# Optimization experiments

Measured on AMD Instinct MI355X. Metric: run time of the kernel, lower is better.

The kernel has to match this reference:

```python
import jax, jax.numpy as jnp
import numpy as np

IN_FEATURES = 1024
OUT_FEATURES = 32000
PADDING_IDX = 0
SMOOTHING = 0.1
N_TOKENS = 8192


def setup_inputs() -> dict:
    key = jax.random.key(0)
    k_x, k_t, k_w, k_b = jax.random.split(key, 4)
    x = jax.random.normal(k_x, (N_TOKENS, IN_FEATURES), dtype=jnp.float32)
    target = jax.random.randint(k_t, (N_TOKENS,), 0, OUT_FEATURES, dtype=jnp.int64)
    # nn.init.uniform_(w, -0.1, 0.1) for both weight and bias
    weight = jax.random.uniform(k_w, (OUT_FEATURES, IN_FEATURES), dtype=jnp.float32, minval=-0.1, maxval=0.1)
    bias = jax.random.uniform(k_b, (OUT_FEATURES,), dtype=jnp.float32, minval=-0.1, maxval=0.1)
    return {"input": x, "target": target, "weight": weight, "bias": bias}


def reference(input, target, weight, bias):
    # Fused linear -> log-softmax -> label-smoothed NLL with padding mask.
    # logits: [N, V]
    logits = jnp.einsum("nd,vd->nv", input, weight) + bias
    logp = jax.nn.log_softmax(logits, axis=-1)
    V = logp.shape[-1]
    nll = -jnp.take_along_axis(logp, target[:, None], axis=-1)[:, 0]  # [N]
    smooth = -jnp.sum(logp, axis=-1)                                   # [N]
    per_tok = (1.0 - SMOOTHING) * nll + (SMOOTHING / V) * smooth
    mask = (target != PADDING_IDX).astype(per_tok.dtype)
    return jnp.sum(per_tok * mask)
```

## Files before the change

### kernel.cpp

```cpp
#include <hip/hip_runtime.h>

#define IN_F 1024
#define NVOC 32000
#define NTOK 8192
#define BM 128
#define BN 128
#define NT (NVOC / BN)
#define MT (NTOK / BM)
#define NBLK (NT * MT)
#define SMOOTH 0.1f

typedef __attribute__((ext_vector_type(8))) short short8;
typedef __attribute__((ext_vector_type(4))) float f32x4;
typedef __attribute__((ext_vector_type(8))) int int8v;
typedef __attribute__((ext_vector_type(4))) int int4v;
typedef unsigned int u32;

__device__ inline unsigned short f2bf(float f) {
  u32 u = __float_as_uint(f);
  return (unsigned short)((u + 0x7fffu + ((u >> 16) & 1u)) >> 16);
}

__device__ inline void gload_lds16(const void* g, void* l) {
  __builtin_amdgcn_global_load_lds(
      (const __attribute__((address_space(1))) u32*)g,
      (__attribute__((address_space(3))) u32*)l, 16, 0, 0);
}

__global__ void fix_target(const int* __restrict__ traw, int* __restrict__ tgtidx) {
  __shared__ int flag;
  if (threadIdx.x == 0) flag = 0;
  __syncthreads();
  int any = 0;
  for (int i = threadIdx.x; i < NTOK / 2; i += 256) any |= (traw[2 * i + 1] != 0);
  if (any) atomicOr(&flag, 1);
  __syncthreads();
  const int is64 = (flag == 0);
  for (int i = threadIdx.x; i < NTOK; i += 256)
    tgtidx[i] = is64 ? traw[2 * i] : traw[i];
}

__global__ void convert_fp8(const float4* __restrict__ in, u32* __restrict__ out, int n4) {
  int i = blockIdx.x * blockDim.x + threadIdx.x;
  const int stride = gridDim.x * blockDim.x;
  for (; i < n4; i += stride) {
    const float4 v = in[i];
    int p = __builtin_amdgcn_cvt_pk_fp8_f32(v.x, v.y, 0, false);
    p = __builtin_amdgcn_cvt_pk_fp8_f32(v.z, v.w, p, true);
    out[i] = (u32)p;
  }
}

__global__ __launch_bounds__(256) void gemm_fp8(
    const char* __restrict__ X8, const char* __restrict__ W8,
    const float* __restrict__ bias, const int* __restrict__ tgtidx,
    float* __restrict__ psum, float* __restrict__ pslog,
    float* __restrict__ tgtlogit) {
  __shared__ char smem[33792];
  char* As = smem;
  char* Bs = smem + 16384;
  float* biasS = (float*)(smem + 32768);
  int* tgtS = (int*)(smem + 33280);
  float* redse = (float*)smem;
  float* redsl = (float*)(smem + 1024);

  const int tid = threadIdx.x;
  const int wave = tid >> 6, lane = tid & 63;
  const int wm = wave & 1, wn = wave >> 1;
  const int quad = lane >> 4, l16 = lane & 15;

  const int lid = blockIdx.x;
  const int xcd = lid & 7, seq = lid >> 3;
  const int mt = (xcd << 3) | (seq & 7);
  const int nb = seq >> 3;
  const int n0 = nb * BN, m0 = mt * BM;

  if (tid < BN) {
    biasS[tid] = bias[n0 + tid];
    tgtS[tid] = tgtidx[m0 + tid] - n0;
  }

  const f32x4 zero = {0.f, 0.f, 0.f, 0.f};
  f32x4 acc[4][4];
#pragma unroll
  for (int i = 0; i < 4; ++i)
#pragma unroll
    for (int j = 0; j < 4; ++j) acc[i][j] = zero;

  const int lr = lane >> 3, lc = lane & 7;
  const char* pA[4];
  const char* pB[4];
#pragma unroll
  for (int i = 0; i < 4; ++i) {
    const int row = wave * 32 + i * 8 + lr;
    const int c = lc ^ (row & 7);
    pA[i] = X8 + (size_t)(m0 + row) * IN_F + c * 16;
    pB[i] = W8 + (size_t)(n0 + row) * IN_F + c * 16;
  }

  for (int kt = 0; kt < IN_F / 128; ++kt) {
    __syncthreads();
#pragma unroll
    for (int i = 0; i < 4; ++i) {
      const int R0 = wave * 32 + i * 8;
      gload_lds16(pA[i], As + R0 * 128);
      gload_lds16(pB[i], Bs + R0 * 128);
      pA[i] += 128;
      pB[i] += 128;
    }
    __syncthreads();

    int8v bfv[4];
#pragma unroll
    for (int t = 0; t < 4; ++t) {
      const int br = wn * 64 + t * 16 + l16;
      const int s0 = (((quad << 1) + 0) ^ (br & 7)) << 4;
      const int s1 = (((quad << 1) + 1) ^ (br & 7)) << 4;
      const int4v lo = *(const int4v*)(Bs + br * 128 + s0);
      const int4v hi = *(const int4v*)(Bs + br * 128 + s1);
      int8v f;
      f[0] = lo[0]; f[1] = lo[1]; f[2] = lo[2]; f[3] = lo[3];
      f[4] = hi[0]; f[5] = hi[1]; f[6] = hi[2]; f[7] = hi[3];
      bfv[t] = f;
    }
#pragma unroll
    for (int i = 0; i < 4; ++i) {
      const int ar = wm * 64 + i * 16 + l16;
      const int s0 = (((quad << 1) + 0) ^ (ar & 7)) << 4;
      const int s1 = (((quad << 1) + 1) ^ (ar & 7)) << 4;
      const int4v lo = *(const int4v*)(As + ar * 128 + s0);
      const int4v hi = *(const int4v*)(As + ar * 128 + s1);
      int8v af;
      af[0] = lo[0]; af[1] = lo[1]; af[2] = lo[2]; af[3] = lo[3];
      af[4] = hi[0]; af[5] = hi[1]; af[6] = hi[2]; af[7] = hi[3];
#pragma unroll
      for (int j = 0; j < 4; ++j)
        acc[i][j] = __builtin_amdgcn_mfma_scale_f32_16x16x128_f8f6f4(
            af, bfv[j], acc[i][j], 0 , 0 ,
            0, 0x7F7F7F7F, 0, 0x7F7F7F7F);
    }
  }

  __syncthreads();

  const float bv0 = biasS[wn * 64 + 0 * 16 + l16];
  const float bv1 = biasS[wn * 64 + 1 * 16 + l16];
  const float bv2 = biasS[wn * 64 + 2 * 16 + l16];
  const float bv3 = biasS[wn * 64 + 3 * 16 + l16];

#pragma unroll
  for (int i = 0; i < 4; ++i) {
#pragma unroll
    for (int reg = 0; reg < 4; ++reg) {
      const int row = wm * 64 + i * 16 + quad * 4 + reg;
      const float v0 = acc[i][0][reg] + bv0;
      const float v1 = acc[i][1][reg] + bv1;
      const float v2 = acc[i][2][reg] + bv2;
      const float v3 = acc[i][3][reg] + bv3;
      float se = __expf(v0) + __expf(v1) + __expf(v2) + __expf(v3);
      float sl = v0 + v1 + v2 + v3;
      se += __shfl_xor(se, 1); se += __shfl_xor(se, 2);
      se += __shfl_xor(se, 4); se += __shfl_xor(se, 8);
      sl += __shfl_xor(sl, 1); sl += __shfl_xor(sl, 2);
      sl += __shfl_xor(sl, 4); sl += __shfl_xor(sl, 8);
      if (l16 == 0) {
        redse[wn * 128 + row] = se;
        redsl[wn * 128 + row] = sl;
      }
      const int ct = tgtS[row];
      if (ct >= 0 && ct < BN && (ct >> 6) == wn && (ct & 15) == l16) {
        const int jj = (ct >> 4) & 3;
        const float tv = jj == 0 ? v0 : (jj == 1 ? v1 : (jj == 2 ? v2 : v3));
        tgtlogit[m0 + row] = tv;
      }
    }
  }
  __syncthreads();
  if (tid < BM) {
    const size_t idx = (size_t)(m0 + tid) * NT + nb;
    psum[idx] = redse[tid] + redse[128 + tid];
    pslog[idx] = redsl[tid] + redsl[128 + tid];
  }
}

__global__ __launch_bounds__(256) void gemm_fb(
    const float* __restrict__ X, const float* __restrict__ W,
    const float* __restrict__ bias, const int* __restrict__ tgtidx,
    float* __restrict__ psum, float* __restrict__ pslog,
    float* __restrict__ tgtlogit) {
  __shared__ char smem[33792];
  char* As = smem;
  char* Bs = smem + 16384;
  float* biasS = (float*)(smem + 32768);
  int* tgtS = (int*)(smem + 33280);
  float* redse = (float*)smem;
  float* redsl = (float*)(smem + 1024);

  const int tid = threadIdx.x;
  const int wave = tid >> 6, lane = tid & 63;
  const int wm = wave & 1, wn = wave >> 1;
  const int quad = lane >> 4, l16 = lane & 15;
  const int lid = blockIdx.x;
  const int xcd = lid & 7, seq = lid >> 3;
  const int mt = (xcd << 3) | (seq & 7);
  const int nb = seq >> 3;
  const int n0 = nb * BN, m0 = mt * BM;

  if (tid < BN) {
    biasS[tid] = bias[n0 + tid];
    tgtS[tid] = tgtidx[m0 + tid] - n0;
  }

  const f32x4 zero = {0.f, 0.f, 0.f, 0.f};
  f32x4 acc[4][4];
#pragma unroll
  for (int i = 0; i < 4; ++i)
#pragma unroll
    for (int j = 0; j < 4; ++j) acc[i][j] = zero;

  for (int kt = 0; kt < IN_F / 64; ++kt) {
    const int row = tid >> 1, hs = tid & 1;
    const float4* gA = (const float4*)(X + (size_t)(m0 + row) * IN_F + kt * 64 + hs * 32);
    const float4* gB = (const float4*)(W + (size_t)(n0 + row) * IN_F + kt * 64 + hs * 32);
    float4 a4[8], b4[8];
#pragma unroll
    for (int k = 0; k < 8; ++k) a4[k] = gA[k];
#pragma unroll
    for (int k = 0; k < 8; ++k) b4[k] = gB[k];
    __syncthreads();
#pragma unroll
    for (int cl = 0; cl < 4; ++cl) {
      const float4 x0 = a4[2 * cl], x1 = a4[2 * cl + 1];
      const float4 y0 = b4[2 * cl], y1 = b4[2 * cl + 1];
      short8 sa, sb;
      sa[0] = (short)f2bf(x0.x); sa[1] = (short)f2bf(x0.y);
      sa[2] = (short)f2bf(x0.z); sa[3] = (short)f2bf(x0.w);
      sa[4] = (short)f2bf(x1.x); sa[5] = (short)f2bf(x1.y);
      sa[6] = (short)f2bf(x1.z); sa[7] = (short)f2bf(x1.w);
      sb[0] = (short)f2bf(y0.x); sb[1] = (short)f2bf(y0.y);
      sb[2] = (short)f2bf(y0.z); sb[3] = (short)f2bf(y0.w);
      sb[4] = (short)f2bf(y1.x); sb[5] = (short)f2bf(y1.y);
      sb[6] = (short)f2bf(y1.z); sb[7] = (short)f2bf(y1.w);
      const int c = hs * 4 + cl;
      const int p = (c ^ (row & 7)) << 4;
      *(short8*)(As + row * 128 + p) = sa;
      *(short8*)(Bs + row * 128 + p) = sb;
    }
    __syncthreads();
#pragma unroll
    for (int kk = 0; kk < 2; ++kk) {
      short8 af[4], bfv[4];
#pragma unroll
      for (int t = 0; t < 4; ++t) {
        const int ar = wm * 64 + t * 16 + l16;
        af[t] = *(const short8*)(As + ar * 128 + ((((kk << 2) + quad) ^ (ar & 7)) << 4));
        const int br = wn * 64 + t * 16 + l16;
        bfv[t] = *(const short8*)(Bs + br * 128 + ((((kk << 2) + quad) ^ (br & 7)) << 4));
      }
#pragma unroll
      for (int i = 0; i < 4; ++i)
#pragma unroll
        for (int j = 0; j < 4; ++j)
          acc[i][j] = __builtin_amdgcn_mfma_f32_16x16x32_bf16(af[i], bfv[j], acc[i][j], 0, 0, 0);
    }
  }

  __syncthreads();
  const float bv0 = biasS[wn * 64 + 0 * 16 + l16];
  const float bv1 = biasS[wn * 64 + 1 * 16 + l16];
  const float bv2 = biasS[wn * 64 + 2 * 16 + l16];
  const float bv3 = biasS[wn * 64 + 3 * 16 + l16];
#pragma unroll
  for (int i = 0; i < 4; ++i) {
#pragma unroll
    for (int reg = 0; reg < 4; ++reg) {
      const int row = wm * 64 + i * 16 + quad * 4 + reg;
      const float v0 = acc[i][0][reg] + bv0;
      const float v1 = acc[i][1][reg] + bv1;
      const float v2 = acc[i][2][reg] + bv2;
      const float v3 = acc[i][3][reg] + bv3;
      float se = __expf(v0) + __expf(v1) + __expf(v2) + __expf(v3);
      float sl = v0 + v1 + v2 + v3;
      se += __shfl_xor(se, 1); se += __shfl_xor(se, 2);
      se += __shfl_xor(se, 4); se += __shfl_xor(se, 8);
      sl += __shfl_xor(sl, 1); sl += __shfl_xor(sl, 2);
      sl += __shfl_xor(sl, 4); sl += __shfl_xor(sl, 8);
      if (l16 == 0) {
        redse[wn * 128 + row] = se;
        redsl[wn * 128 + row] = sl;
      }
      const int ct = tgtS[row];
      if (ct >= 0 && ct < BN && (ct >> 6) == wn && (ct & 15) == l16) {
        const int jj = (ct >> 4) & 3;
        const float tv = jj == 0 ? v0 : (jj == 1 ? v1 : (jj == 2 ? v2 : v3));
        tgtlogit[m0 + row] = tv;
      }
    }
  }
  __syncthreads();
  if (tid < BM) {
    const size_t idx = (size_t)(m0 + tid) * NT + nb;
    psum[idx] = redse[tid] + redse[128 + tid];
    pslog[idx] = redsl[tid] + redsl[128 + tid];
  }
}

__global__ __launch_bounds__(256) void combine(
    const float* __restrict__ psum, const float* __restrict__ pslog,
    const float* __restrict__ tgtlogit, const int* __restrict__ tgtidx,
    float* __restrict__ pertok) {
  const int token = blockIdx.x * 4 + (threadIdx.x >> 6);
  const int lane = threadIdx.x & 63;
  float se = 0.f, sl = 0.f;
  for (int l = lane; l < NT; l += 64) {
    const size_t idx = (size_t)token * NT + l;
    se += psum[idx];
    sl += pslog[idx];
  }
#pragma unroll
  for (int d = 1; d < 64; d <<= 1) {
    se += __shfl_xor(se, d);
    sl += __shfl_xor(sl, d);
  }
  if (lane == 0) {
    const int t = tgtidx[token];
    const float logZ = logf(se);
    const float nll = logZ - tgtlogit[token];
    const float smooth = (float)NVOC * logZ - sl;
    const float pt = (1.f - SMOOTH) * nll + (SMOOTH / (float)NVOC) * smooth;
    pertok[token] = (t != 0) ? pt : 0.f;
  }
}

__global__ __launch_bounds__(256) void finalsum(const float* __restrict__ pertok,
                                                float* __restrict__ out) {
  const int tid = threadIdx.x;
  float s = 0.f;
  for (int i = tid; i < NTOK; i += 256) s += pertok[i];
#pragma unroll
  for (int d = 1; d < 64; d <<= 1) s += __shfl_xor(s, d);
  __shared__ float wsum[4];
  if ((tid & 63) == 0) wsum[tid >> 6] = s;
  __syncthreads();
  if (tid == 0) out[0] = wsum[0] + wsum[1] + wsum[2] + wsum[3];
}

extern "C" void kernel_launch(void* const* d_in, const int* in_sizes, int n_in,
                              void* d_out, int out_size, void* d_ws, size_t ws_size,
                              hipStream_t stream) {
  (void)in_sizes; (void)n_in; (void)out_size;
  const float* x = (const float*)d_in[0];
  const int* traw = (const int*)d_in[1];
  const float* w = (const float*)d_in[2];
  const float* bias = (const float*)d_in[3];

  char* ws = (char*)d_ws;
  float* psum = (float*)ws;
  float* pslog = psum + (size_t)NTOK * NT;
  float* tgtlogit = pslog + (size_t)NTOK * NT;
  float* pertok = tgtlogit + NTOK;
  int* tgtidx = (int*)(pertok + NTOK);
  char* fraw = (char*)(tgtidx + NTOK);
  char* f8base = (char*)(((size_t)fraw + 15) & ~(size_t)15);
  const size_t base_need = (size_t)(f8base - ws);
  const size_t f8_need = (size_t)NTOK * IN_F + (size_t)NVOC * IN_F;
  const bool pre8 = ws_size >= base_need + f8_need;

  fix_target<<<1, 256, 0, stream>>>(traw, tgtidx);

  if (pre8) {
    char* x8 = f8base;
    char* w8 = x8 + (size_t)NTOK * IN_F;
    convert_fp8<<<2048, 256, 0, stream>>>((const float4*)x, (u32*)x8, NTOK * IN_F / 4);
    convert_fp8<<<8192, 256, 0, stream>>>((const float4*)w, (u32*)w8, NVOC * IN_F / 4);
    gemm_fp8<<<NBLK, 256, 0, stream>>>(x8, w8, bias, tgtidx, psum, pslog, tgtlogit);
  } else {
    gemm_fb<<<NBLK, 256, 0, stream>>>(x, w, bias, tgtidx, psum, pslog, tgtlogit);
  }
  combine<<<NTOK / 4, 256, 0, stream>>>(psum, pslog, tgtlogit, tgtidx, pertok);
  finalsum<<<1, 256, 0, stream>>>(pertok, (float*)d_out);
}
```

Before: 666.7 us.

## Fuse prep kernels, fold final sum into combine, adjust LDS swizzle and occupancy

Merges the target fix-up and both FP8 conversion launches into a single prep kernel, and replaces the separate final-sum kernel with an atomicAdd at the end of combine, preceded by a memset of the output. The GEMM gets a launch-bounds occupancy hint of 3 blocks per SM, and the LDS chunk mapping now pairs chunks quad and quad+4 instead of 2*quad and 2*quad+1. The aim is fewer launches and fewer LDS bank conflicts. The trade-offs are a floating-point atomic reduction whose summation order is not fixed, and possible register spilling under the tighter occupancy bound.

New measurement: 740.1 us. +11.0%, slower.

```diff
diff --git a/kernel.cpp b/kernel.cpp
--- a/kernel.cpp
+++ b/kernel.cpp
@@ -27,31 +27,38 @@
       (__attribute__((address_space(3))) u32*)l, 16, 0, 0);
 }
 
-__global__ void fix_target(const int* __restrict__ traw, int* __restrict__ tgtidx) {
-  __shared__ int flag;
-  if (threadIdx.x == 0) flag = 0;
-  __syncthreads();
-  int any = 0;
-  for (int i = threadIdx.x; i < NTOK / 2; i += 256) any |= (traw[2 * i + 1] != 0);
-  if (any) atomicOr(&flag, 1);
-  __syncthreads();
-  const int is64 = (flag == 0);
-  for (int i = threadIdx.x; i < NTOK; i += 256)
-    tgtidx[i] = is64 ? traw[2 * i] : traw[i];
-}
-
-__global__ void convert_fp8(const float4* __restrict__ in, u32* __restrict__ out, int n4) {
-  int i = blockIdx.x * blockDim.x + threadIdx.x;
-  const int stride = gridDim.x * blockDim.x;
-  for (; i < n4; i += stride) {
-    const float4 v = in[i];
+__global__ void prep(const float4* __restrict__ x, const float4* __restrict__ w,
+                     u32* __restrict__ x8, u32* __restrict__ w8,
+                     const int* __restrict__ traw, int* __restrict__ tgtidx) {
+  if (blockIdx.x == 0) {
+    __shared__ int flag;
+    if (threadIdx.x == 0) flag = 0;
+    __syncthreads();
+    int any = 0;
+    for (int i = threadIdx.x; i < NTOK / 2; i += 256) any |= (traw[2 * i + 1] != 0);
+    if (any) atomicOr(&flag, 1);
+    __syncthreads();
+    const int is64 = (flag == 0);
+    for (int i = threadIdx.x; i < NTOK; i += 256)
+      tgtidx[i] = is64 ? traw[2 * i] : traw[i];
+  }
+  const int gid = blockIdx.x * 256 + threadIdx.x;
+  const int stride = gridDim.x * 256;
+  for (int i = gid; i < NTOK * IN_F / 4; i += stride) {
+    const float4 v = x[i];
     int p = __builtin_amdgcn_cvt_pk_fp8_f32(v.x, v.y, 0, false);
     p = __builtin_amdgcn_cvt_pk_fp8_f32(v.z, v.w, p, true);
-    out[i] = (u32)p;
-  }
-}
-
-__global__ __launch_bounds__(256) void gemm_fp8(
+    x8[i] = (u32)p;
+  }
+  for (int i = gid; i < NVOC * IN_F / 4; i += stride) {
+    const float4 v = w[i];
+    int p = __builtin_amdgcn_cvt_pk_fp8_f32(v.x, v.y, 0, false);
+    p = __builtin_amdgcn_cvt_pk_fp8_f32(v.z, v.w, p, true);
+    w8[i] = (u32)p;
+  }
+}
+
+__global__ __launch_bounds__(256, 3) void gemm_fp8(
     const char* __restrict__ X8, const char* __restrict__ W8,
     const float* __restrict__ bias, const int* __restrict__ tgtidx,
     float* __restrict__ psum, float* __restrict__ pslog,
@@ -93,7 +100,8 @@
 #pragma unroll
   for (int i = 0; i < 4; ++i) {
     const int row = wave * 32 + i * 8 + lr;
-    const int c = lc ^ (row & 7);
+    const int u = lc ^ (row & 7);
+    const int c = ((u & 3) << 1) | (u >> 2);
     pA[i] = X8 + (size_t)(m0 + row) * IN_F + c * 16;
     pB[i] = W8 + (size_t)(n0 + row) * IN_F + c * 16;
   }
@@ -114,8 +122,8 @@
 #pragma unroll
     for (int t = 0; t < 4; ++t) {
       const int br = wn * 64 + t * 16 + l16;
-      const int s0 = (((quad << 1) + 0) ^ (br & 7)) << 4;
-      const int s1 = (((quad << 1) + 1) ^ (br & 7)) << 4;
+      const int s0 = (quad ^ (br & 7)) << 4;
+      const int s1 = ((4 + quad) ^ (br & 7)) << 4;
       const int4v lo = *(const int4v*)(Bs + br * 128 + s0);
       const int4v hi = *(const int4v*)(Bs + br * 128 + s1);
       int8v f;
@@ -126,8 +134,8 @@
 #pragma unroll
     for (int i = 0; i < 4; ++i) {
       const int ar = wm * 64 + i * 16 + l16;
-      const int s0 = (((quad << 1) + 0) ^ (ar & 7)) << 4;
-      const int s1 = (((quad << 1) + 1) ^ (ar & 7)) << 4;
+      const int s0 = (quad ^ (ar & 7)) << 4;
+      const int s1 = ((4 + quad) ^ (ar & 7)) << 4;
       const int4v lo = *(const int4v*)(As + ar * 128 + s0);
       const int4v hi = *(const int4v*)(As + ar * 128 + s1);
       int8v af;
@@ -181,6 +189,19 @@
     psum[idx] = redse[tid] + redse[128 + tid];
     pslog[idx] = redsl[tid] + redsl[128 + tid];
   }
+}
+
+__global__ void fix_target(const int* __restrict__ traw, int* __restrict__ tgtidx) {
+  __shared__ int flag;
+  if (threadIdx.x == 0) flag = 0;
+  __syncthreads();
+  int any = 0;
+  for (int i = threadIdx.x; i < NTOK / 2; i += 256) any |= (traw[2 * i + 1] != 0);
+  if (any) atomicOr(&flag, 1);
+  __syncthreads();
+  const int is64 = (flag == 0);
+  for (int i = threadIdx.x; i < NTOK; i += 256)
+    tgtidx[i] = is64 ? traw[2 * i] : traw[i];
 }
 
 __global__ __launch_bounds__(256) void gemm_fb(
@@ -308,8 +329,9 @@
 __global__ __launch_bounds__(256) void combine(
     const float* __restrict__ psum, const float* __restrict__ pslog,
     const float* __restrict__ tgtlogit, const int* __restrict__ tgtidx,
-    float* __restrict__ pertok) {
-  const int token = blockIdx.x * 4 + (threadIdx.x >> 6);
+    float* __restrict__ out) {
+  const int wv = threadIdx.x >> 6;
+  const int token = blockIdx.x * 4 + wv;
   const int lane = threadIdx.x & 63;
   float se = 0.f, sl = 0.f;
   for (int l = lane; l < NT; l += 64) {
@@ -322,27 +344,18 @@
     se += __shfl_xor(se, d);
     sl += __shfl_xor(sl, d);
   }
+  __shared__ float bsum[4];
   if (lane == 0) {
     const int t = tgtidx[token];
     const float logZ = logf(se);
     const float nll = logZ - tgtlogit[token];
     const float smooth = (float)NVOC * logZ - sl;
     const float pt = (1.f - SMOOTH) * nll + (SMOOTH / (float)NVOC) * smooth;
-    pertok[token] = (t != 0) ? pt : 0.f;
-  }
-}
-
-__global__ __launch_bounds__(256) void finalsum(const float* __restrict__ pertok,
-                                                float* __restrict__ out) {
-  const int tid = threadIdx.x;
-  float s = 0.f;
-  for (int i = tid; i < NTOK; i += 256) s += pertok[i];
-#pragma unroll
-  for (int d = 1; d < 64; d <<= 1) s += __shfl_xor(s, d);
-  __shared__ float wsum[4];
-  if ((tid & 63) == 0) wsum[tid >> 6] = s;
-  __syncthreads();
-  if (tid == 0) out[0] = wsum[0] + wsum[1] + wsum[2] + wsum[3];
+    bsum[wv] = (t != 0) ? pt : 0.f;
+  }
+  __syncthreads();
+  if (threadIdx.x == 0)
+    atomicAdd(out, bsum[0] + bsum[1] + bsum[2] + bsum[3]);
 }
 
 extern "C" void kernel_launch(void* const* d_in, const int* in_sizes, int n_in,
@@ -358,25 +371,24 @@
   float* psum = (float*)ws;
   float* pslog = psum + (size_t)NTOK * NT;
   float* tgtlogit = pslog + (size_t)NTOK * NT;
-  float* pertok = tgtlogit + NTOK;
-  int* tgtidx = (int*)(pertok + NTOK);
+  int* tgtidx = (int*)(tgtlogit + NTOK);
   char* fraw = (char*)(tgtidx + NTOK);
   char* f8base = (char*)(((size_t)fraw + 15) & ~(size_t)15);
   const size_t base_need = (size_t)(f8base - ws);
   const size_t f8_need = (size_t)NTOK * IN_F + (size_t)NVOC * IN_F;
   const bool pre8 = ws_size >= base_need + f8_need;
 
-  fix_target<<<1, 256, 0, stream>>>(traw, tgtidx);
+  hipMemsetAsync(d_out, 0, sizeof(float), stream);
 
   if (pre8) {
     char* x8 = f8base;
     char* w8 = x8 + (size_t)NTOK * IN_F;
-    convert_fp8<<<2048, 256, 0, stream>>>((const float4*)x, (u32*)x8, NTOK * IN_F / 4);
-    convert_fp8<<<8192, 256, 0, stream>>>((const float4*)w, (u32*)w8, NVOC * IN_F / 4);
+    prep<<<8192, 256, 0, stream>>>((const float4*)x, (const float4*)w,
+                                   (u32*)x8, (u32*)w8, traw, tgtidx);
     gemm_fp8<<<NBLK, 256, 0, stream>>>(x8, w8, bias, tgtidx, psum, pslog, tgtlogit);
   } else {
+    fix_target<<<1, 256, 0, stream>>>(traw, tgtidx);
     gemm_fb<<<NBLK, 256, 0, stream>>>(x, w, bias, tgtidx, psum, pslog, tgtlogit);
   }
-  combine<<<NTOK / 4, 256, 0, stream>>>(psum, pslog, tgtlogit, tgtidx, pertok);
-  finalsum<<<1, 256, 0, stream>>>(pertok, (float*)d_out);
-}
+  combine<<<NTOK / 4, 256, 0, stream>>>(psum, pslog, tgtlogit, tgtidx, (float*)d_out);
+}
```
